# Performance work log

Hardware: AMD Instinct MI355X
Metric: run time of the kernel (lower is better)

Reference implementation:

```python
import jax, jax.numpy as jnp
import numpy as np

RATIO = 2
KSIZE = 12
PAD = KSIZE // 2 - RATIO // 2  # 5


def setup_inputs() -> dict:
    key = jax.random.key(0)
    k1, k2 = jax.random.split(key)
    x = jax.random.normal(k1, (4, 64, 256, 256), dtype=jnp.float32)
    # fixed anti-aliasing filter buffer (kaiser-jinc in original); random stand-in
    filt = jax.random.normal(k2, (KSIZE, KSIZE), dtype=jnp.float32)
    return {"x": x, "filt": filt}


def reference(x, filt):
    B, C, H, W = x.shape
    # reflect pad
    xp = jnp.pad(x, ((0, 0), (0, 0), (PAD, PAD), (PAD, PAD)), mode="reflect")
    # depthwise conv_transpose2d(stride=RATIO, groups=C) == conv with
    # lhs_dilation=RATIO, full padding (k-1), spatially flipped kernel
    w = jnp.broadcast_to(filt[::-1, ::-1][None, None], (C, 1, KSIZE, KSIZE))
    y = jax.lax.conv_general_dilated(
        xp, w,
        window_strides=(1, 1),
        padding=[(KSIZE - 1, KSIZE - 1)] * 2,
        lhs_dilation=(RATIO, RATIO),
        dimension_numbers=("NCHW", "OIHW", "NCHW"),
        feature_group_count=C,
    )
    y = (RATIO ** 2) * y
    pl = PAD * RATIO + (KSIZE - RATIO) // 2       # 15
    pr = PAD * RATIO + (KSIZE - RATIO + 1) // 2   # 15
    return y[..., pl:-pr, pl:-pr]
```

## Files before the change

### kernel.cpp

```cpp
#include <hip/hip_runtime.h>


#define S 40
#define WREG (14 * S)

__global__ __launch_bounds__(256) void upsample2d_kernel(
    const float* __restrict__ x, const float* __restrict__ filt,
    float* __restrict__ out)
{
    __shared__ float s_in[4 * WREG];

    const int tx = threadIdx.x, ty = threadIdx.y;
    const int w    = ty >> 2;
    const int lane = (ty & 3) * 16 + tx;
    const int bc  = blockIdx.z;
    const int boy = blockIdx.y, box = blockIdx.x;

    const float* xc = x + (size_t)bc * 65536;

    float* sw = s_in + w * WREG;
    const int row0 = boy * 32 + w * 8 - 3;
    const int col0 = box * 32 - 3;
    #pragma unroll
    for (int k = 0; k < 9; ++k) {
        int idx = lane + k * 64;
        if (idx > 531) idx = 531;
        int r = (idx * 1725) >> 16;
        int c = idx - r * 38;
        int gy = row0 + r, gx = col0 + c;
        gy = gy < 0 ? -gy : (gy > 255 ? 510 - gy : gy);
        gx = gx < 0 ? -gx : (gx > 255 ? 510 - gx : gx);
        sw[r * S + c] = xc[gy * 256 + gx];
    }

    const int xb = w * WREG + (2 * (ty & 3)) * S + 2 * tx;
    float xr[8][8];
    #pragma unroll
    for (int r = 0; r < 8; ++r) {
        #pragma unroll
        for (int cc = 0; cc < 8; ++cc)
            xr[r][cc] = s_in[xb + r * S + cc];
    }

    float acc[4][4] = {};
    #pragma unroll
    for (int py = 0; py < 2; ++py)
    #pragma unroll
    for (int px = 0; px < 2; ++px) {
        #pragma unroll
        for (int m = 0; m < 6; ++m)
        #pragma unroll
        for (int n = 0; n < 6; ++n) {
            const float f = filt[(11 - py - 2 * m) * 12 + (11 - px - 2 * n)];
            #pragma unroll
            for (int qy = 0; qy < 2; ++qy)
            #pragma unroll
            for (int qx = 0; qx < 2; ++qx)
                acc[2 * qy + py][2 * qx + px] =
                    fmaf(xr[qy + py + m][qx + px + n], f,
                         acc[2 * qy + py][2 * qx + px]);
        }
    }

    float* oc = out + (size_t)bc * 262144;
    const int OY0 = boy * 64 + 4 * ty;
    const int OX  = box * 64 + 4 * tx;
    #pragma unroll
    for (int oy = 0; oy < 4; ++oy) {
        float4 v = make_float4(4.0f * acc[oy][0], 4.0f * acc[oy][1],
                               4.0f * acc[oy][2], 4.0f * acc[oy][3]);
        *reinterpret_cast<float4*>(&oc[(size_t)(OY0 + oy) * 512 + OX]) = v;
    }
}

extern "C" void kernel_launch(void* const* d_in, const int* in_sizes, int n_in,
                              void* d_out, int out_size, void* d_ws, size_t ws_size,
                              hipStream_t stream) {
    const float* x    = (const float*)d_in[0];
    const float* filt = (const float*)d_in[1];
    float* out = (float*)d_out;

    dim3 grid(8, 8, 256);
    dim3 block(16, 16, 1);
    upsample2d_kernel<<<grid, block, 0, stream>>>(x, filt, out);
}
```

Baseline: 92.03 us.

## Load input tile via global_load_lds and stream rows to cut registers

Input tile loads now go straight from global memory into LDS with the global_load_lds builtin instead of through registers. Each warp's region widens to 576 floats so the 40-column rows map onto 64-lane chunks. The compute loop is reordered to load one 8-element input row at a time instead of holding an 8x8 register array, and launch bounds ask for 8 blocks per SM to raise occupancy. The risks are more filter loads from global or constant memory inside the reordered loop, and possible register spills under the tighter bound.

```diff
diff --git a/kernel.cpp b/kernel.cpp
--- a/kernel.cpp
+++ b/kernel.cpp
@@ -2,9 +2,12 @@
 
 
 #define S 40
-#define WREG (14 * S)
+#define WREG 576
 
-__global__ __launch_bounds__(256) void upsample2d_kernel(
+typedef __attribute__((address_space(3))) void lds_t;
+typedef __attribute__((address_space(1))) const void gm_t;
+
+__global__ __launch_bounds__(256, 8) void upsample2d_kernel(
     const float* __restrict__ x, const float* __restrict__ filt,
     float* __restrict__ out)
 {
@@ -17,48 +20,48 @@
     const int boy = blockIdx.y, box = blockIdx.x;
 
     const float* xc = x + (size_t)bc * 65536;
+    const int row0 = boy * 32 + w * 8 - 3;
+    const int col0 = box * 32 - 3;
 
     float* sw = s_in + w * WREG;
-    const int row0 = boy * 32 + w * 8 - 3;
-    const int col0 = box * 32 - 3;
+
     #pragma unroll
     for (int k = 0; k < 9; ++k) {
-        int idx = lane + k * 64;
-        if (idx > 531) idx = 531;
-        int r = (idx * 1725) >> 16;
-        int c = idx - r * 38;
+        int j = lane + 64 * k;
+        int r = (j * 1639) >> 16;
+        int c = j - r * 40;
         int gy = row0 + r, gx = col0 + c;
-        gy = gy < 0 ? -gy : (gy > 255 ? 510 - gy : gy);
-        gx = gx < 0 ? -gx : (gx > 255 ? 510 - gx : gx);
-        sw[r * S + c] = xc[gy * 256 + gx];
+        gy = gy < 0 ? -gy : gy;  gy = gy > 255 ? 510 - gy : gy;
+        gx = gx < 0 ? -gx : gx;  gx = gx > 255 ? 510 - gx : gx;
+        __builtin_amdgcn_global_load_lds((gm_t*)(xc + gy * 256 + gx),
+                                         (lds_t*)(sw + 64 * k), 4, 0, 0);
     }
+    asm volatile("s_waitcnt vmcnt(0)" ::: "memory");
 
     const int xb = w * WREG + (2 * (ty & 3)) * S + 2 * tx;
-    float xr[8][8];
+    float acc[4][4] = {};
     #pragma unroll
     for (int r = 0; r < 8; ++r) {
+        float xrr[8];
         #pragma unroll
-        for (int cc = 0; cc < 8; ++cc)
-            xr[r][cc] = s_in[xb + r * S + cc];
-    }
-
-    float acc[4][4] = {};
-    #pragma unroll
-    for (int py = 0; py < 2; ++py)
-    #pragma unroll
-    for (int px = 0; px < 2; ++px) {
+        for (int cc = 0; cc < 8; ++cc) xrr[cc] = s_in[xb + r * S + cc];
         #pragma unroll
-        for (int m = 0; m < 6; ++m)
+        for (int qy = 0; qy < 2; ++qy)
         #pragma unroll
-        for (int n = 0; n < 6; ++n) {
-            const float f = filt[(11 - py - 2 * m) * 12 + (11 - px - 2 * n)];
-            #pragma unroll
-            for (int qy = 0; qy < 2; ++qy)
-            #pragma unroll
-            for (int qx = 0; qx < 2; ++qx)
-                acc[2 * qy + py][2 * qx + px] =
-                    fmaf(xr[qy + py + m][qx + px + n], f,
-                         acc[2 * qy + py][2 * qx + px]);
+        for (int py = 0; py < 2; ++py) {
+            const int m = r - qy - py;
+            if (m >= 0 && m <= 5) {
+                #pragma unroll
+                for (int px = 0; px < 2; ++px)
+                #pragma unroll
+                for (int n = 0; n < 6; ++n) {
+                    const float f = filt[(11 - py - 2 * m) * 12 + (11 - px - 2 * n)];
+                    #pragma unroll
+                    for (int qx = 0; qx < 2; ++qx)
+                        acc[2 * qy + py][2 * qx + px] =
+                            fmaf(xrr[qx + px + n], f, acc[2 * qy + py][2 * qx + px]);
+                }
+            }
         }
     }
 
```

Result: no change. 91.93 us (-0.1%).
